# Kernel optimization log

Hardware: AMD Instinct MI355X
Metric: run time of the kernel (lower is better)

Reference implementation:

```python
import jax, jax.numpy as jnp
import numpy as np

N, IN, HID, OUT, HEADS, E = 50000, 256, 128, 128, 2, 800000
NEG_SLOPE = 0.2


def gat_conv(x, edge_src, edge_dst, W, att_src, att_dst, bias):
    # x: [N, F_in]; W: [F_in, H*C]; att_*: [H, C]; bias: [C]
    n = x.shape[0]
    H, C = att_src.shape
    xl = (x @ W).reshape(n, H, C)                       # [N, H, C]
    a_src = jnp.sum(xl * att_src, axis=-1)              # [N, H]
    a_dst = jnp.sum(xl * att_dst, axis=-1)              # [N, H]
    e = jax.nn.leaky_relu(a_src[edge_src] + a_dst[edge_dst], NEG_SLOPE)  # [E+N, H]
    e_max = jax.ops.segment_max(e, edge_dst, num_segments=n)            # [N, H]
    e = jnp.exp(e - e_max[edge_dst])
    denom = jax.ops.segment_sum(e, edge_dst, num_segments=n)            # [N, H]
    alpha = e / (denom[edge_dst] + 1e-16)                               # [E+N, H]
    msg = xl[edge_src] * alpha[:, :, None]                              # [E+N, H, C]
    out = jax.ops.segment_sum(msg, edge_dst, num_segments=n)            # [N, H, C]
    return out.mean(axis=1) + bias                                      # concat=False: head mean


def setup_inputs() -> dict:
    key = jax.random.key(0)
    ks = jax.random.split(key, 12)
    x = jax.random.normal(ks[0], (N, IN), dtype=jnp.float32)
    edge_index = jax.random.randint(ks[1], (2, E), 0, N, dtype=jnp.int64)
    s = 0.1
    W0 = jax.random.normal(ks[2], (IN, HEADS * HID), dtype=jnp.float32) * s
    att_src0 = jax.random.normal(ks[3], (HEADS, HID), dtype=jnp.float32) * s
    att_dst0 = jax.random.normal(ks[4], (HEADS, HID), dtype=jnp.float32) * s
    bias0 = jnp.zeros((HID,), dtype=jnp.float32)
    W1 = jax.random.normal(ks[5], (HID, HEADS * HID), dtype=jnp.float32) * s
    att_src1 = jax.random.normal(ks[6], (HEADS, HID), dtype=jnp.float32) * s
    att_dst1 = jax.random.normal(ks[7], (HEADS, HID), dtype=jnp.float32) * s
    bias1 = jnp.zeros((HID,), dtype=jnp.float32)
    proj_w = jax.random.normal(ks[8], (HID, OUT), dtype=jnp.float32) * s
    proj_b = jnp.zeros((OUT,), dtype=jnp.float32)
    return {"x": x, "edge_index": edge_index,
            "W0": W0, "att_src0": att_src0, "att_dst0": att_dst0, "bias0": bias0,
            "W1": W1, "att_src1": att_src1, "att_dst1": att_dst1, "bias1": bias1,
            "proj_w": proj_w, "proj_b": proj_b}


def reference(x, edge_index, W0, att_src0, att_dst0, bias0, W1, att_src1, att_dst1, bias1, proj_w, proj_b):
    n = x.shape[0]
    loops = jnp.arange(n, dtype=edge_index.dtype)
    # PyG GATConv default add_self_loops=True
    src = jnp.concatenate([edge_index[0], loops])
    dst = jnp.concatenate([edge_index[1], loops])
    h = gat_conv(x, src, dst, W0, att_src0, att_dst0, bias0)
    h = jax.nn.gelu(h, approximate=False)
    h = gat_conv(h, src, dst, W1, att_src1, att_dst1, bias1)
    h = jax.nn.gelu(h, approximate=False)
    return h @ proj_w + proj_b
```

## Files before the change

### kernel.cpp

```cpp
#include <hip/hip_runtime.h>
#include <math.h>


#define NEG_SLOPE 0.2f

typedef __attribute__((ext_vector_type(8))) short bf16x8;
typedef __attribute__((ext_vector_type(8))) ushort u16x8;
typedef __attribute__((ext_vector_type(4))) float f32x4;

__device__ __forceinline__ void split_f32(float x, ushort& h, ushort& l)
{
    unsigned b = __float_as_uint(x);
    h = (ushort)(b >> 16);
    float xh = __uint_as_float(b & 0xffff0000u);
    l = (ushort)(__float_as_uint(x - xh) >> 16);
}

__device__ __forceinline__ ushort f32_to_bf16_rne(float x)
{
    unsigned u = __float_as_uint(x);
    return (ushort)((u + 0x7fffu + ((u >> 16) & 1u)) >> 16);
}

__device__ __forceinline__ float bf16_to_f32(ushort u)
{
    return __uint_as_float(((unsigned)u) << 16);
}

__device__ __forceinline__ float lrelu(float x)
{
    return x > 0.f ? x : NEG_SLOPE * x;
}

__device__ __forceinline__ float gelu_exact(float x)
{
    return 0.5f * x * (1.0f + erff(x * 0.7071067811865476f));
}

__global__ __launch_bounds__(256)
void prep_kernel(const float* __restrict__ W0, const float* __restrict__ W1,
                 const float* __restrict__ PW,
                 const float* __restrict__ as0, const float* __restrict__ ad0,
                 const float* __restrict__ as1, const float* __restrict__ ad1,
                 ushort* __restrict__ w0h, ushort* __restrict__ w0l,
                 ushort* __restrict__ w1h, ushort* __restrict__ w1l,
                 ushort* __restrict__ pwh, ushort* __restrict__ pwl,
                 float* __restrict__ wt0, float* __restrict__ wt1)
{
    const int blk = blockIdx.x;
    if (blk < 448) {
        int t = blk * 256 + threadIdx.x;
        ushort h, l;
        if (t < 65536) {
            int k = t >> 8, n = t & 255;
            split_f32(W0[t], h, l);
            w0h[n * 256 + k] = h; w0l[n * 256 + k] = l;
        } else if (t < 65536 + 32768) {
            int u = t - 65536;
            int k = u >> 8, n = u & 255;
            split_f32(W1[u], h, l);
            w1h[n * 128 + k] = h; w1l[n * 128 + k] = l;
        } else {
            int u = t - 65536 - 32768;
            int k = u >> 7, n = u & 127;
            split_f32(PW[u], h, l);
            pwh[n * 128 + k] = h; pwl[n * 128 + k] = l;
        }
        return;
    }
    const float *W, *as_, *ad_;
    float* wt;
    int k;
    if (blk < 704) { W = W0; as_ = as0; ad_ = ad0; wt = wt0; k = blk - 448; }
    else           { W = W1; as_ = as1; ad_ = ad1; wt = wt1; k = blk - 704; }

    const int t = threadIdx.x;
    const int h = t >> 7, c = t & 127;
    const int lane = t & 63, wid = t >> 6;
    const float w = W[(size_t)k * 256 + h * 128 + c];
    float ps = w * as_[h * 128 + c];
    float pd = w * ad_[h * 128 + c];
#pragma unroll
    for (int off = 1; off < 64; off <<= 1) {
        ps += __shfl_xor(ps, off, 64);
        pd += __shfl_xor(pd, off, 64);
    }
    __shared__ float sm[4][2];
    if (lane == 0) { sm[wid][0] = ps; sm[wid][1] = pd; }
    __syncthreads();
    if (t == 0) {
        wt[k * 4 + 0] = sm[0][0] + sm[1][0];
        wt[k * 4 + 1] = sm[2][0] + sm[3][0];
        wt[k * 4 + 2] = sm[0][1] + sm[1][1];
        wt[k * 4 + 3] = sm[2][1] + sm[3][1];
    }
}

__global__ __launch_bounds__(256)
void attn_matvec_kernel(const float* __restrict__ X,
                        const float* __restrict__ watt,
                        float* __restrict__ a_s, float* __restrict__ a_d,
                        int n, int K)
{
    const int wave = threadIdx.x >> 6;
    const int lane = threadIdx.x & 63;
    const int v = blockIdx.x * 4 + wave;
    if (v >= n) return;

    float s0 = 0.f, s1 = 0.f, d0 = 0.f, d1 = 0.f;
    const int k0 = lane << 2;
    if (k0 < K) {
        const float4 xv = *(const float4*)(X + (size_t)v * K + k0);
        const float x4[4] = {xv.x, xv.y, xv.z, xv.w};
#pragma unroll
        for (int i = 0; i < 4; ++i) {
            const float4 wv = *(const float4*)(watt + (k0 + i) * 4);
            s0 += x4[i] * wv.x;
            s1 += x4[i] * wv.y;
            d0 += x4[i] * wv.z;
            d1 += x4[i] * wv.w;
        }
    }
#pragma unroll
    for (int off = 1; off < 64; off <<= 1) {
        s0 += __shfl_xor(s0, off, 64);
        s1 += __shfl_xor(s1, off, 64);
        d0 += __shfl_xor(d0, off, 64);
        d1 += __shfl_xor(d1, off, 64);
    }
    if (lane == 0) {
        *(float2*)(a_s + (size_t)v * 2) = make_float2(s0, s1);
        *(float2*)(a_d + (size_t)v * 2) = make_float2(d0, d1);
    }
}

template<int BN, bool SPLITA>
__global__ __launch_bounds__(512)
void mfma_gemm3(const float* __restrict__ Af,
                const ushort* __restrict__ Aio,
                const ushort* __restrict__ Bth, const ushort* __restrict__ Btl,
                const float* __restrict__ bias,
                float* __restrict__ Cf, ushort* __restrict__ Cb,
                int M, int K)
{
    constexpr int NF = BN / 64;
    __shared__ ushort Ah[4][128][8];
    __shared__ ushort Al[4][128][8];
    __shared__ ushort Bh[4][BN][8];
    __shared__ ushort Bl[4][BN][8];

    const int tid = threadIdx.x;
    const int r0 = blockIdx.x * 128;
    const int w = tid >> 6, lane = tid & 63;
    const int wr = (w & 1) * 64;
    const int wc = (w >> 1) * (BN / 4);
    const int lr = lane & 15, kb = lane >> 4;

    const int arow = tid >> 2;
    const int apl = tid & 3;

    f32x4 acc[4][NF] = {};

    for (int kk = 0; kk < K; kk += 32) {
        {
            const int row = r0 + arow;
            u16x8 h0 = {}, l0 = {};
            if (row < M) {
                if constexpr (SPLITA) {
                    const float* p = Af + (size_t)row * K + kk + apl * 8;
                    float4 v0 = *(const float4*)(p);
                    float4 v1 = *(const float4*)(p + 4);
                    float va[8] = {v0.x, v0.y, v0.z, v0.w, v1.x, v1.y, v1.z, v1.w};
#pragma unroll
                    for (int i = 0; i < 8; ++i) {
                        ushort hh_, ll_;
                        split_f32(va[i], hh_, ll_);
                        h0[i] = hh_; l0[i] = ll_;
                    }
                } else {
                    const ushort* p = Aio + (size_t)row * (2 * K) + kk + apl * 8;
                    h0 = *(const u16x8*)(p);
                    l0 = *(const u16x8*)(p + K);
                }
            }
            *(u16x8*)&Ah[apl][arow][0] = h0;
            *(u16x8*)&Al[apl][arow][0] = l0;
        }
        if constexpr (BN == 256) {
            const int col = tid >> 1, half = tid & 1;
            const ushort* ph = Bth + (size_t)col * K + kk + half * 16;
            const ushort* pl = Btl + (size_t)col * K + kk + half * 16;
            *(u16x8*)&Bh[half * 2 + 0][col][0] = *(const u16x8*)(ph);
            *(u16x8*)&Bh[half * 2 + 1][col][0] = *(const u16x8*)(ph + 8);
            *(u16x8*)&Bl[half * 2 + 0][col][0] = *(const u16x8*)(pl);
            *(u16x8*)&Bl[half * 2 + 1][col][0] = *(const u16x8*)(pl + 8);
        } else {
            const int col = tid >> 2, pl = tid & 3;
            *(u16x8*)&Bh[pl][col][0] = *(const u16x8*)(Bth + (size_t)col * K + kk + pl * 8);
            *(u16x8*)&Bl[pl][col][0] = *(const u16x8*)(Btl + (size_t)col * K + kk + pl * 8);
        }
        __syncthreads();

        bf16x8 ah[4], al[4];
#pragma unroll
        for (int m = 0; m < 4; ++m) {
            ah[m] = *(const bf16x8*)&Ah[kb][wr + m * 16 + lr][0];
            al[m] = *(const bf16x8*)&Al[kb][wr + m * 16 + lr][0];
        }
#pragma unroll
        for (int n = 0; n < NF; ++n) {
            const bf16x8 bh = *(const bf16x8*)&Bh[kb][wc + n * 16 + lr][0];
            const bf16x8 bl = *(const bf16x8*)&Bl[kb][wc + n * 16 + lr][0];
#pragma unroll
            for (int m = 0; m < 4; ++m) {
                acc[m][n] = __builtin_amdgcn_mfma_f32_16x16x32_bf16(ah[m], bh, acc[m][n], 0, 0, 0);
                acc[m][n] = __builtin_amdgcn_mfma_f32_16x16x32_bf16(ah[m], bl, acc[m][n], 0, 0, 0);
                acc[m][n] = __builtin_amdgcn_mfma_f32_16x16x32_bf16(al[m], bh, acc[m][n], 0, 0, 0);
            }
        }
        __syncthreads();
    }

#pragma unroll
    for (int n = 0; n < NF; ++n) {
        const int col = wc + n * 16 + lr;
        const float bv = bias ? bias[col] : 0.f;
#pragma unroll
        for (int m = 0; m < 4; ++m) {
            const int rowb = r0 + wr + m * 16 + kb * 4;
#pragma unroll
            for (int j = 0; j < 4; ++j) {
                const int row = rowb + j;
                if (row < M) {
                    const float val = acc[m][n][j] + bv;
                    if (Cf) Cf[(size_t)row * BN + col] = val;
                    if (Cb) Cb[(size_t)row * BN + col] = f32_to_bf16_rne(val);
                }
            }
        }
    }
}

__global__ __launch_bounds__(256)
void gat_gather_kernel(const ushort* __restrict__ xlb,
                       const int* __restrict__ rowptr,
                       const int* __restrict__ esrc,
                       const float* __restrict__ a_si,
                       const float* __restrict__ a_di,
                       const float* __restrict__ bias,
                       const float* __restrict__ watt,
                       float* __restrict__ a_so, float* __restrict__ a_do,
                       ushort* __restrict__ outio,
                       int n)
{
    const int wave = threadIdx.x >> 6;
    const int lane = threadIdx.x & 63;
    const int v = blockIdx.x * 4 + wave;
    if (v >= n) return;
    const int h = lane >> 5;
    const int j0 = lane & 31;
    const int c4 = j0 << 2;

    const float adv = a_di[v * 2 + h];
    const float wself = __expf(lrelu(a_si[v * 2 + h] + adv));

    const ushort4 xv4 = *(const ushort4*)(xlb + (size_t)v * 256 + (lane << 2));
    float4 acc0, acc1;
    acc0.x = wself * bf16_to_f32(xv4.x);
    acc0.y = wself * bf16_to_f32(xv4.y);
    acc0.z = wself * bf16_to_f32(xv4.z);
    acc0.w = wself * bf16_to_f32(xv4.w);
    acc1 = make_float4(0.f, 0.f, 0.f, 0.f);
    float ssum = (j0 == 0) ? wself : 0.f;

    const int beg = rowptr[v], end = rowptr[v + 1];
    for (int i = beg; i < end; i += 32) {
        const int cnt = min(32, end - i);
        int myidx = 0;
        float myw = 0.f;
        if (j0 < cnt) {
            myidx = esrc[i + j0];
            myw = __expf(lrelu(a_si[myidx * 2 + h] + adv));
        }
        ssum += myw;
#pragma unroll 2
        for (int j = 0; j < cnt; ++j) {
            const int src = __builtin_amdgcn_readlane(myidx, j);
            const float wgt = __shfl(myw, j, 32);
            const ushort4 xs4 = *(const ushort4*)(xlb + (size_t)src * 256 + (lane << 2));
            if (j & 1) {
                acc1.x += wgt * bf16_to_f32(xs4.x);
                acc1.y += wgt * bf16_to_f32(xs4.y);
                acc1.z += wgt * bf16_to_f32(xs4.z);
                acc1.w += wgt * bf16_to_f32(xs4.w);
            } else {
                acc0.x += wgt * bf16_to_f32(xs4.x);
                acc0.y += wgt * bf16_to_f32(xs4.y);
                acc0.z += wgt * bf16_to_f32(xs4.z);
                acc0.w += wgt * bf16_to_f32(xs4.w);
            }
        }
    }

#pragma unroll
    for (int off = 1; off < 32; off <<= 1)
        ssum += __shfl_xor(ssum, off, 64);
    const float inv = 1.0f / (ssum + 1e-16f);

    float4 r;
    r.x = (acc0.x + acc1.x) * inv;
    r.y = (acc0.y + acc1.y) * inv;
    r.z = (acc0.z + acc1.z) * inv;
    r.w = (acc0.w + acc1.w) * inv;
    float4 o;
    o.x = 0.5f * (r.x + __shfl_xor(r.x, 32, 64));
    o.y = 0.5f * (r.y + __shfl_xor(r.y, 32, 64));
    o.z = 0.5f * (r.z + __shfl_xor(r.z, 32, 64));
    o.w = 0.5f * (r.w + __shfl_xor(r.w, 32, 64));

    const float4 bb = *(const float4*)(bias + c4);
    o.x = gelu_exact(o.x + bb.x);
    o.y = gelu_exact(o.y + bb.y);
    o.z = gelu_exact(o.z + bb.z);
    o.w = gelu_exact(o.w + bb.w);

    if (watt) {
        const float ov[4] = {o.x, o.y, o.z, o.w};
        float s0 = 0.f, s1 = 0.f, d0 = 0.f, d1 = 0.f;
#pragma unroll
        for (int i = 0; i < 4; ++i) {
            const float4 wv = *(const float4*)(watt + (c4 + i) * 4);
            s0 += ov[i] * wv.x;
            s1 += ov[i] * wv.y;
            d0 += ov[i] * wv.z;
            d1 += ov[i] * wv.w;
        }
#pragma unroll
        for (int off = 1; off < 64; off <<= 1) {
            s0 += __shfl_xor(s0, off, 64);
            s1 += __shfl_xor(s1, off, 64);
            d0 += __shfl_xor(d0, off, 64);
            d1 += __shfl_xor(d1, off, 64);
        }
        if (lane == 0) {
            *(float2*)(a_so + (size_t)v * 2) = make_float2(0.5f * s0, 0.5f * s1);
            *(float2*)(a_do + (size_t)v * 2) = make_float2(0.5f * d0, 0.5f * d1);
        }
    }

    ushort4 st;
    ushort hh_, ll_;
    split_f32(o.x, hh_, ll_); st.x = (lane < 32) ? hh_ : ll_;
    split_f32(o.y, hh_, ll_); st.y = (lane < 32) ? hh_ : ll_;
    split_f32(o.z, hh_, ll_); st.z = (lane < 32) ? hh_ : ll_;
    split_f32(o.w, hh_, ll_); st.w = (lane < 32) ? hh_ : ll_;
    *(ushort4*)(outio + (size_t)v * 256 + (lane << 2)) = st;
}

__global__ __launch_bounds__(256)
void hist_kernel(const int* __restrict__ ei, int* __restrict__ cnt, int E)
{
    int e = blockIdx.x * 256 + threadIdx.x;
    if (e < E) atomicAdd(&cnt[ei[E + e]], 1);
}

__global__ __launch_bounds__(256)
void blocksum_kernel(const int* __restrict__ cnt, int* __restrict__ bsum, int n)
{
    __shared__ int sm[256];
    const int t = threadIdx.x;
    const int i = blockIdx.x * 256 + t;
    sm[t] = (i < n) ? cnt[i] : 0;
    __syncthreads();
#pragma unroll
    for (int off = 1; off < 256; off <<= 1) {
        int u = (t >= off) ? sm[t - off] : 0;
        __syncthreads();
        sm[t] += u;
        __syncthreads();
    }
    if (t == 255) bsum[blockIdx.x] = sm[255];
}

__global__ __launch_bounds__(256)
void scan_bsum_kernel(int* __restrict__ bsum, int nb, int* __restrict__ ptr, int n)
{
    __shared__ int sm[256];
    const int t = threadIdx.x;
    const int v = (t < nb) ? bsum[t] : 0;
    sm[t] = v;
    __syncthreads();
#pragma unroll
    for (int off = 1; off < 256; off <<= 1) {
        int u = (t >= off) ? sm[t - off] : 0;
        __syncthreads();
        sm[t] += u;
        __syncthreads();
    }
    if (t < nb) bsum[t] = sm[t] - v;
    if (t == 255) ptr[n] = sm[255];
}

__global__ __launch_bounds__(256)
void scan_out_kernel(const int* __restrict__ cnt, const int* __restrict__ bsum,
                     int* __restrict__ ptr, int* __restrict__ pcur, int n)
{
    __shared__ int sm[256];
    const int t = threadIdx.x;
    const int i = blockIdx.x * 256 + t;
    const int v = (i < n) ? cnt[i] : 0;
    sm[t] = v;
    __syncthreads();
#pragma unroll
    for (int off = 1; off < 256; off <<= 1) {
        int u = (t >= off) ? sm[t - off] : 0;
        __syncthreads();
        sm[t] += u;
        __syncthreads();
    }
    if (i < n) {
        const int val = bsum[blockIdx.x] + sm[t] - v;
        ptr[i] = val;
        pcur[i] = val;
    }
}

__global__ __launch_bounds__(256)
void scatter_kernel(const int* __restrict__ ei, int* __restrict__ pcur,
                    int* __restrict__ esrc, int E)
{
    int e = blockIdx.x * 256 + threadIdx.x;
    if (e < E) {
        int dst = ei[E + e];
        int src = ei[e];
        int pos = atomicAdd(&pcur[dst], 1);
        esrc[pos] = src;
    }
}

extern "C" void kernel_launch(void* const* d_in, const int* in_sizes, int n_in,
                              void* d_out, int out_size, void* d_ws, size_t ws_size,
                              hipStream_t stream)
{
    const float* x       = (const float*)d_in[0];
    const int*   ei      = (const int*)d_in[1];
    const float* W0      = (const float*)d_in[2];
    const float* att_s0  = (const float*)d_in[3];
    const float* att_d0  = (const float*)d_in[4];
    const float* b0      = (const float*)d_in[5];
    const float* W1      = (const float*)d_in[6];
    const float* att_s1  = (const float*)d_in[7];
    const float* att_d1  = (const float*)d_in[8];
    const float* b1      = (const float*)d_in[9];
    const float* pw      = (const float*)d_in[10];
    const float* pb      = (const float*)d_in[11];

    const int N = in_sizes[0] / 256;
    const int E = in_sizes[1] / 2;
    const int NB = (N + 255) / 256;

    ushort* xlb  = (ushort*)d_ws;
    ushort* hio  = xlb + (size_t)N * 256;
    float*  a_s  = (float*)(hio + (size_t)N * 256);
    float*  a_d  = a_s + (size_t)N * 2;
    float*  a_s2 = a_d + (size_t)N * 2;
    float*  a_d2 = a_s2 + (size_t)N * 2;
    float*  wt0  = a_d2 + (size_t)N * 2;
    float*  wt1  = wt0 + 256 * 4;
    int*    cnt  = (int*)(wt1 + 128 * 4);
    int*    ptr  = cnt + N;
    int*    pcur = ptr + (N + 1);
    int*    bsm  = pcur + N;
    int*    esr  = bsm + 256;
    ushort* w0h  = (ushort*)(esr + E);
    ushort* w0l  = w0h + 256 * 256;
    ushort* w1h  = w0l + 256 * 256;
    ushort* w1l  = w1h + 256 * 128;
    ushort* pwh  = w1l + 256 * 128;
    ushort* pwl  = pwh + 128 * 128;

    const int ablk = (N + 3) / 4;
    const int eblk = (E + 255) / 256;
    const int gblk = (N + 127) / 128;

    prep_kernel<<<832, 256, 0, stream>>>(
        W0, W1, pw, att_s0, att_d0, att_s1, att_d1,
        w0h, w0l, w1h, w1l, pwh, pwl, wt0, wt1);

    hipMemsetAsync(cnt, 0, (size_t)N * sizeof(int), stream);
    hist_kernel<<<eblk, 256, 0, stream>>>(ei, cnt, E);
    blocksum_kernel<<<NB, 256, 0, stream>>>(cnt, bsm, N);
    scan_bsum_kernel<<<1, 256, 0, stream>>>(bsm, NB, ptr, N);
    scan_out_kernel<<<NB, 256, 0, stream>>>(cnt, bsm, ptr, pcur, N);
    scatter_kernel<<<eblk, 256, 0, stream>>>(ei, pcur, esr, E);

    mfma_gemm3<256, true><<<gblk, 512, 0, stream>>>(
        x, nullptr, w0h, w0l, nullptr, nullptr, xlb, N, 256);
    attn_matvec_kernel<<<ablk, 256, 0, stream>>>(x, wt0, a_s, a_d, N, 256);
    gat_gather_kernel<<<ablk, 256, 0, stream>>>(
        xlb, ptr, esr, a_s, a_d, b0, wt1, a_s2, a_d2, hio, N);

    mfma_gemm3<256, false><<<gblk, 512, 0, stream>>>(
        nullptr, hio, w1h, w1l, nullptr, nullptr, xlb, N, 128);
    gat_gather_kernel<<<ablk, 256, 0, stream>>>(
        xlb, ptr, esr, a_s2, a_d2, b1, nullptr, nullptr, nullptr, hio, N);

    mfma_gemm3<128, false><<<gblk, 512, 0, stream>>>(
        nullptr, hio, pwh, pwl, pb, (float*)d_out, nullptr, N, 128);
}
```

Before: 354.5 us.

## Fuse layer-0 attention score computation into GEMM epilogue and fold memset into prep

Removes the separate attention matvec kernel, which re-read the full x matrix. Layer-0 attention logits are now computed from the fp32 GEMM accumulators via a block-diagonal att vector, reduced with wave shuffles and shared memory. The count-buffer memset is folded into the prep kernel as extra blocks, saving one launch. The cost is extra epilogue work and a block sync inside the GEMM, which reuses the A tile's shared memory after the main loop. It also changes summation order slightly, since xl is now formed before the attention dot product.

```diff
diff --git a/kernel.cpp b/kernel.cpp
--- a/kernel.cpp
+++ b/kernel.cpp
@@ -45,9 +45,23 @@
                  ushort* __restrict__ w0h, ushort* __restrict__ w0l,
                  ushort* __restrict__ w1h, ushort* __restrict__ w1l,
                  ushort* __restrict__ pwh, ushort* __restrict__ pwl,
-                 float* __restrict__ wt0, float* __restrict__ wt1)
+                 float* __restrict__ wtd0, float* __restrict__ wt1,
+                 int* __restrict__ cnt, int N)
 {
     const int blk = blockIdx.x;
+    if (blk >= 577) {
+        int t2 = (blk - 577) * 256 + threadIdx.x;
+        if (t2 < N) cnt[t2] = 0;
+        return;
+    }
+    if (blk == 576) {
+        const int col = threadIdx.x;
+        float4 o;
+        if (col < 128) o = make_float4(as0[col], 0.f, ad0[col], 0.f);
+        else           o = make_float4(0.f, as0[col], 0.f, ad0[col]);
+        *(float4*)(wtd0 + col * 4) = o;
+        return;
+    }
     if (blk < 448) {
         int t = blk * 256 + threadIdx.x;
         ushort h, l;
@@ -68,18 +82,13 @@
         }
         return;
     }
-    const float *W, *as_, *ad_;
-    float* wt;
-    int k;
-    if (blk < 704) { W = W0; as_ = as0; ad_ = ad0; wt = wt0; k = blk - 448; }
-    else           { W = W1; as_ = as1; ad_ = ad1; wt = wt1; k = blk - 704; }
-
+    const int k = blk - 448;
     const int t = threadIdx.x;
     const int h = t >> 7, c = t & 127;
     const int lane = t & 63, wid = t >> 6;
-    const float w = W[(size_t)k * 256 + h * 128 + c];
-    float ps = w * as_[h * 128 + c];
-    float pd = w * ad_[h * 128 + c];
+    const float w = W1[(size_t)k * 256 + h * 128 + c];
+    float ps = w * as1[h * 128 + c];
+    float pd = w * ad1[h * 128 + c];
 #pragma unroll
     for (int off = 1; off < 64; off <<= 1) {
         ps += __shfl_xor(ps, off, 64);
@@ -89,48 +98,10 @@
     if (lane == 0) { sm[wid][0] = ps; sm[wid][1] = pd; }
     __syncthreads();
     if (t == 0) {
-        wt[k * 4 + 0] = sm[0][0] + sm[1][0];
-        wt[k * 4 + 1] = sm[2][0] + sm[3][0];
-        wt[k * 4 + 2] = sm[0][1] + sm[1][1];
-        wt[k * 4 + 3] = sm[2][1] + sm[3][1];
-    }
-}
-
-__global__ __launch_bounds__(256)
-void attn_matvec_kernel(const float* __restrict__ X,
-                        const float* __restrict__ watt,
-                        float* __restrict__ a_s, float* __restrict__ a_d,
-                        int n, int K)
-{
-    const int wave = threadIdx.x >> 6;
-    const int lane = threadIdx.x & 63;
-    const int v = blockIdx.x * 4 + wave;
-    if (v >= n) return;
-
-    float s0 = 0.f, s1 = 0.f, d0 = 0.f, d1 = 0.f;
-    const int k0 = lane << 2;
-    if (k0 < K) {
-        const float4 xv = *(const float4*)(X + (size_t)v * K + k0);
-        const float x4[4] = {xv.x, xv.y, xv.z, xv.w};
-#pragma unroll
-        for (int i = 0; i < 4; ++i) {
-            const float4 wv = *(const float4*)(watt + (k0 + i) * 4);
-            s0 += x4[i] * wv.x;
-            s1 += x4[i] * wv.y;
-            d0 += x4[i] * wv.z;
-            d1 += x4[i] * wv.w;
-        }
-    }
-#pragma unroll
-    for (int off = 1; off < 64; off <<= 1) {
-        s0 += __shfl_xor(s0, off, 64);
-        s1 += __shfl_xor(s1, off, 64);
-        d0 += __shfl_xor(d0, off, 64);
-        d1 += __shfl_xor(d1, off, 64);
-    }
-    if (lane == 0) {
-        *(float2*)(a_s + (size_t)v * 2) = make_float2(s0, s1);
-        *(float2*)(a_d + (size_t)v * 2) = make_float2(d0, d1);
+        wt1[k * 4 + 0] = sm[0][0] + sm[1][0];
+        wt1[k * 4 + 1] = sm[2][0] + sm[3][0];
+        wt1[k * 4 + 2] = sm[0][1] + sm[1][1];
+        wt1[k * 4 + 3] = sm[2][1] + sm[3][1];
     }
 }
 
@@ -141,6 +112,8 @@
                 const ushort* __restrict__ Bth, const ushort* __restrict__ Btl,
                 const float* __restrict__ bias,
                 float* __restrict__ Cf, ushort* __restrict__ Cb,
+                const float* __restrict__ watt,
+                float* __restrict__ a_sc, float* __restrict__ a_dc,
                 int M, int K)
 {
     constexpr int NF = BN / 64;
@@ -237,6 +210,52 @@
                     if (Cb) Cb[(size_t)row * BN + col] = f32_to_bf16_rne(val);
                 }
             }
+        }
+    }
+
+    if (watt) {
+        float* sp = (float*)&Ah[0][0][0];
+        float4 wv[NF];
+#pragma unroll
+        for (int n = 0; n < NF; ++n)
+            wv[n] = *(const float4*)(watt + (wc + n * 16 + lr) * 4);
+#pragma unroll
+        for (int m = 0; m < 4; ++m) {
+#pragma unroll
+            for (int j = 0; j < 4; ++j) {
+                float s0 = 0.f, s1 = 0.f, s2 = 0.f, s3 = 0.f;
+#pragma unroll
+                for (int n = 0; n < NF; ++n) {
+                    const float v = acc[m][n][j];
+                    s0 += v * wv[n].x;
+                    s1 += v * wv[n].y;
+                    s2 += v * wv[n].z;
+                    s3 += v * wv[n].w;
+                }
+#pragma unroll
+                for (int off = 1; off < 16; off <<= 1) {
+                    s0 += __shfl_xor(s0, off, 64);
+                    s1 += __shfl_xor(s1, off, 64);
+                    s2 += __shfl_xor(s2, off, 64);
+                    s3 += __shfl_xor(s3, off, 64);
+                }
+                if (lr == 0) {
+                    const int row = wr + m * 16 + kb * 4 + j;
+                    float* d = sp + ((w >> 1) * 128 + row) * 4;
+                    d[0] = s0; d[1] = s1; d[2] = s2; d[3] = s3;
+                }
+            }
+        }
+        __syncthreads();
+        const int row = tid >> 2, comp = tid & 3;
+        const float s = sp[(0 * 128 + row) * 4 + comp]
+                      + sp[(1 * 128 + row) * 4 + comp]
+                      + sp[(2 * 128 + row) * 4 + comp]
+                      + sp[(3 * 128 + row) * 4 + comp];
+        const int gr = r0 + row;
+        if (gr < M) {
+            if (comp < 2) a_sc[(size_t)gr * 2 + comp] = s;
+            else          a_dc[(size_t)gr * 2 + (comp - 2)] = s;
         }
     }
 }
@@ -465,8 +484,8 @@
     float*  a_d  = a_s + (size_t)N * 2;
     float*  a_s2 = a_d + (size_t)N * 2;
     float*  a_d2 = a_s2 + (size_t)N * 2;
-    float*  wt0  = a_d2 + (size_t)N * 2;
-    float*  wt1  = wt0 + 256 * 4;
+    float*  wtd0 = a_d2 + (size_t)N * 2;
+    float*  wt1  = wtd0 + 256 * 4;
     int*    cnt  = (int*)(wt1 + 128 * 4);
     int*    ptr  = cnt + N;
     int*    pcur = ptr + (N + 1);
@@ -483,11 +502,10 @@
     const int eblk = (E + 255) / 256;
     const int gblk = (N + 127) / 128;
 
-    prep_kernel<<<832, 256, 0, stream>>>(
+    prep_kernel<<<577 + NB, 256, 0, stream>>>(
         W0, W1, pw, att_s0, att_d0, att_s1, att_d1,
-        w0h, w0l, w1h, w1l, pwh, pwl, wt0, wt1);
-
-    hipMemsetAsync(cnt, 0, (size_t)N * sizeof(int), stream);
+        w0h, w0l, w1h, w1l, pwh, pwl, wtd0, wt1, cnt, N);
+
     hist_kernel<<<eblk, 256, 0, stream>>>(ei, cnt, E);
     blocksum_kernel<<<NB, 256, 0, stream>>>(cnt, bsm, N);
     scan_bsum_kernel<<<1, 256, 0, stream>>>(bsm, NB, ptr, N);
@@ -495,16 +513,15 @@
     scatter_kernel<<<eblk, 256, 0, stream>>>(ei, pcur, esr, E);
 
     mfma_gemm3<256, true><<<gblk, 512, 0, stream>>>(
-        x, nullptr, w0h, w0l, nullptr, nullptr, xlb, N, 256);
-    attn_matvec_kernel<<<ablk, 256, 0, stream>>>(x, wt0, a_s, a_d, N, 256);
+        x, nullptr, w0h, w0l, nullptr, nullptr, xlb, wtd0, a_s, a_d, N, 256);
     gat_gather_kernel<<<ablk, 256, 0, stream>>>(
         xlb, ptr, esr, a_s, a_d, b0, wt1, a_s2, a_d2, hio, N);
 
     mfma_gemm3<256, false><<<gblk, 512, 0, stream>>>(
-        nullptr, hio, w1h, w1l, nullptr, nullptr, xlb, N, 128);
+        nullptr, hio, w1h, w1l, nullptr, nullptr, xlb, nullptr, nullptr, nullptr, N, 128);
     gat_gather_kernel<<<ablk, 256, 0, stream>>>(
         xlb, ptr, esr, a_s2, a_d2, b1, nullptr, nullptr, nullptr, hio, N);
 
     mfma_gemm3<128, false><<<gblk, 512, 0, stream>>>(
-        nullptr, hio, pwh, pwl, pb, (float*)d_out, nullptr, N, 128);
-}
+        nullptr, hio, pwh, pwl, pb, (float*)d_out, nullptr, nullptr, nullptr, nullptr, N, 128);
+}
```

Measured after the change: 346.1 us. 2.4% less time.
